# Kernel optimization log

Hardware: AMD Instinct MI355X
Metric: run time of the kernel (lower is better)

## Reference

```python
import jax, jax.numpy as jnp
import numpy as np

N_NODES = 100000
N_EDGES = 1600000
VOCAB = 128
D = 30
N_CLASSES = 5


def setup_inputs() -> dict:
    key = jax.random.key(0)
    ks = jax.random.split(key, 8)
    x = jax.random.randint(ks[0], (N_NODES,), 0, VOCAB)
    edge_index = jax.random.randint(ks[1], (2, N_EDGES), 0, N_NODES)
    emb = jax.random.normal(ks[2], (VOCAB, D), dtype=jnp.float32)
    W1 = jax.random.normal(ks[3], (D, D), dtype=jnp.float32) * (1.0 / np.sqrt(D))
    W2 = jax.random.normal(ks[4], (D, D), dtype=jnp.float32) * (1.0 / np.sqrt(D))
    W3 = jax.random.normal(ks[5], (D, D), dtype=jnp.float32) * (1.0 / np.sqrt(D))
    Wout = jax.random.normal(ks[6], (N_CLASSES, D), dtype=jnp.float32) * (1.0 / np.sqrt(D))
    b1 = jnp.zeros((D,), jnp.float32)
    b2 = jnp.zeros((D,), jnp.float32)
    b3 = jnp.zeros((D,), jnp.float32)
    bout = jnp.zeros((N_CLASSES,), jnp.float32)
    return dict(x=x, edge_index=edge_index, emb=emb, W1=W1, b1=b1, W2=W2, b2=b2,
                W3=W3, b3=b3, Wout=Wout, bout=bout)


def _gnn_layer(h, row, col, W, b):
    # h: [N, D]; row/col: [E+N] (self loops appended)
    n = h.shape[0]
    deg = jax.ops.segment_sum(jnp.ones(row.shape, h.dtype), row, num_segments=n)  # [N]
    msg = h[row] / deg[row][:, None]                 # gather + normalize: [E+N, D]
    agg = jax.ops.segment_sum(msg, col, num_segments=n)  # scatter-add: [N, D]
    return jax.nn.relu(agg @ W.T + b)


def reference(x, edge_index, emb, W1, b1, W2, b2, W3, b3, Wout, bout):
    n = x.shape[0]
    loops = jnp.arange(n, dtype=edge_index.dtype)
    row = jnp.concatenate([edge_index[0], loops])  # add_self_loops
    col = jnp.concatenate([edge_index[1], loops])
    h = emb[x]  # [N, D]
    for W, b in ((W1, b1), (W2, b2), (W3, b3)):
        h = _gnn_layer(h, row, col, W, b)
    return h @ Wout.T + bout  # [N, 5]
```

## Files before the change

### kernel.cpp

```cpp
#include <hip/hip_runtime.h>

#define D 30
#define DP 32
#define NCLS 5
#define VOCAB 128
#define BS 256
#define BSHIFT 8
#define BNODES 256
#define NSBMAX 512
#define CAP 8192
#define NBLK_S 256
#define CHUNK 6272
#define LDSCAP 6144
#define NPB 32


__global__ void k_init(int* __restrict__ gcur, int* __restrict__ rcur, int nsb) {
    int i = blockIdx.x * blockDim.x + threadIdx.x;
    if (i < nsb) { gcur[i] = i * CAP; rcur[i] = i * CAP; }
}

__global__ void __launch_bounds__(BS)
k_scatter3(const int* __restrict__ row, const int* __restrict__ col,
           int* __restrict__ gcur, int* __restrict__ rcur,
           int* __restrict__ ebuf, unsigned char* __restrict__ rbuf,
           int e, int nsb) {
    __shared__ int pay[CHUNK];
    __shared__ unsigned short bof[CHUNK];
    __shared__ int lhist[NSBMAX];
    __shared__ int lscan[NSBMAX];
    __shared__ int lcur[NSBMAX];
    __shared__ int gdst[NSBMAX];
    unsigned char* pay8 = (unsigned char*)pay;

    int per = (e + NBLK_S - 1) / NBLK_S;
    int s = blockIdx.x * per; if (s > e) s = e;
    int t = s + per; if (t > e) t = e;
    int m = t - s;
    int tid = threadIdx.x;

    for (int phase = 0; phase < 2; ++phase) {
        const int* key = phase == 0 ? col : row;
        lhist[tid] = 0; lhist[tid + 256] = 0;
        __syncthreads();
        for (int i = s + tid; i < t; i += BS)
            atomicAdd(&lhist[key[i] >> BSHIFT], 1);
        __syncthreads();
        lscan[tid] = lhist[tid]; lscan[tid + 256] = lhist[tid + 256];
        __syncthreads();
        for (int st = 1; st < NSBMAX; st <<= 1) {
            int t0 = (tid >= st) ? lscan[tid - st] : 0;
            int t1 = (tid + 256 >= st) ? lscan[tid + 256 - st] : 0;
            __syncthreads();
            lscan[tid] += t0; lscan[tid + 256] += t1;
            __syncthreads();
        }
        lcur[tid] = lscan[tid] - lhist[tid];
        lcur[tid + 256] = lscan[tid + 256] - lhist[tid + 256];
        __syncthreads();
        if (phase == 0) {
            for (int i = s + tid; i < t; i += BS) {
                int c = col[i], b = c >> BSHIFT;
                int p = atomicAdd(&lcur[b], 1);
                pay[p] = (row[i] << BSHIFT) | (c & (BNODES - 1));
                bof[p] = (unsigned short)b;
            }
        } else {
            for (int i = s + tid; i < t; i += BS) {
                int r = row[i], b = r >> BSHIFT;
                int p = atomicAdd(&lcur[b], 1);
                pay8[p] = (unsigned char)(r & (BNODES - 1));
                bof[p] = (unsigned short)b;
            }
        }
        __syncthreads();
        int* cur = phase == 0 ? gcur : rcur;
        for (int b = tid; b < nsb; b += BS) {
            int h = lhist[b];
            gdst[b] = h ? atomicAdd(&cur[b], h) : 0;
        }
        __syncthreads();
        if (phase == 0) {
            for (int p = tid; p < m; p += BS) {
                int b = bof[p];
                ebuf[gdst[b] + (p - (lscan[b] - lhist[b]))] = pay[p];
            }
        } else {
            for (int p = tid; p < m; p += BS) {
                int b = bof[p];
                rbuf[gdst[b] + (p - (lscan[b] - lhist[b]))] = pay8[p];
            }
        }
        __syncthreads();
    }
}

__global__ void __launch_bounds__(BS)
k_odbsort(int* __restrict__ ebuf, const unsigned char* __restrict__ rbuf,
          const int* __restrict__ gcur, const int* __restrict__ rcur,
          const int* __restrict__ x, float* __restrict__ rdeg, int2* __restrict__ xr,
          int* __restrict__ off, int* __restrict__ cnt, int n) {
    __shared__ int ledge[LDSCAP];
    __shared__ int c256[BNODES];
    __shared__ int b256[BNODES];
    __shared__ int cur256[BNODES];
    int bkt = blockIdx.x;
    int tid = threadIdx.x;
    int base = bkt * CAP;
    int rm = rcur[bkt] - base;
    c256[tid] = 0;
    __syncthreads();
    for (int k = tid; k < rm; k += BS)
        atomicAdd(&c256[rbuf[base + k]], 1);
    __syncthreads();
    {
        int node = (bkt << BSHIFT) + tid;
        if (node < n) {
            float rd = 1.0f / (float)(c256[tid] + 1);
            rdeg[node] = rd;
            xr[node] = make_int2(x[node], __float_as_int(rd));
        }
    }
    __syncthreads();
    int m = gcur[bkt] - base;
    if (m > LDSCAP) m = LDSCAP;
    for (int k = tid; k < m; k += BS) ledge[k] = ebuf[base + k];
    c256[tid] = 0;
    __syncthreads();
    for (int k = tid; k < m; k += BS)
        atomicAdd(&c256[ledge[k] & (BNODES - 1)], 1);
    __syncthreads();
    b256[tid] = c256[tid];
    __syncthreads();
    for (int st = 1; st < BNODES; st <<= 1) {
        int tv = (tid >= st) ? b256[tid - st] : 0;
        __syncthreads();
        b256[tid] += tv;
        __syncthreads();
    }
    cur256[tid] = b256[tid] - c256[tid];
    {
        int node = (bkt << BSHIFT) + tid;
        if (node < n) {
            off[node] = base + b256[tid] - c256[tid];
            cnt[node] = c256[tid];
        }
    }
    __syncthreads();
    for (int k = tid; k < m; k += BS) {
        int v = ledge[k];
        int p = atomicAdd(&cur256[v & (BNODES - 1)], 1);
        ebuf[base + p] = v >> BSHIFT;
    }
}

__global__ void k_prep_emb(const float* __restrict__ emb, float* __restrict__ embp) {
    int tid = blockIdx.x * blockDim.x + threadIdx.x;
    if (tid >= VOCAB * DP) return;
    int v = tid >> 5, c = tid & (DP - 1);
    embp[tid] = (c < D) ? emb[v * D + c] : 0.0f;
}

__global__ void __launch_bounds__(BS)
k_agg_lin(const float* __restrict__ Ain, const int2* __restrict__ xr,
          const float* __restrict__ embp,
          const int* __restrict__ off, const int* __restrict__ cnt,
          const int* __restrict__ esrc, const float* __restrict__ rdeg,
          const float* __restrict__ W, const float* __restrict__ bias,
          const float* __restrict__ Wout, const float* __restrict__ bout,
          float* __restrict__ Aout, float* __restrict__ out,
          int n, int srcmode, int outmode) {
    __shared__ float aggS[NPB * DP];
    __shared__ float h3S[NPB * D];
    __shared__ float Ws[D * D];
    __shared__ float bs_[D];
    __shared__ float WoS[NCLS * D];
    __shared__ float boS[NCLS];
    const float4* Ain4  = (const float4*)Ain;
    const float4* embp4 = (const float4*)embp;
    int i0 = blockIdx.x * NPB;
    int j = threadIdx.x >> 3;
    int q = threadIdx.x & 7;
    int i = i0 + j;
    for (int p = threadIdx.x; p < D * D; p += BS) Ws[p] = W[p];
    if (threadIdx.x < D) bs_[threadIdx.x] = bias[threadIdx.x];
    if (outmode == 1) {
        for (int p = threadIdx.x; p < NCLS * D; p += BS) WoS[p] = Wout[p];
        if (threadIdx.x < NCLS) boS[threadIdx.x] = bout[threadIdx.x];
    }
    float ax = 0.0f, ay = 0.0f, az = 0.0f, aw = 0.0f;
    if (i < n) {
        int base = off[i], c = cnt[i], k = 0;
        if (srcmode == 0) {
            float4 sv = Ain4[(size_t)i * 8 + q];
            ax = sv.x; ay = sv.y; az = sv.z; aw = sv.w;
            for (; k + 8 <= c; k += 8) {
                int s0 = esrc[base + k + 0], s1 = esrc[base + k + 1];
                int s2 = esrc[base + k + 2], s3 = esrc[base + k + 3];
                int s4 = esrc[base + k + 4], s5 = esrc[base + k + 5];
                int s6 = esrc[base + k + 6], s7 = esrc[base + k + 7];
                float4 a0 = Ain4[(size_t)s0 * 8 + q];
                float4 a1 = Ain4[(size_t)s1 * 8 + q];
                float4 a2 = Ain4[(size_t)s2 * 8 + q];
                float4 a3 = Ain4[(size_t)s3 * 8 + q];
                float4 a4 = Ain4[(size_t)s4 * 8 + q];
                float4 a5 = Ain4[(size_t)s5 * 8 + q];
                float4 a6 = Ain4[(size_t)s6 * 8 + q];
                float4 a7 = Ain4[(size_t)s7 * 8 + q];
                ax += a0.x; ay += a0.y; az += a0.z; aw += a0.w;
                ax += a1.x; ay += a1.y; az += a1.z; aw += a1.w;
                ax += a2.x; ay += a2.y; az += a2.z; aw += a2.w;
                ax += a3.x; ay += a3.y; az += a3.z; aw += a3.w;
                ax += a4.x; ay += a4.y; az += a4.z; aw += a4.w;
                ax += a5.x; ay += a5.y; az += a5.z; aw += a5.w;
                ax += a6.x; ay += a6.y; az += a6.z; aw += a6.w;
                ax += a7.x; ay += a7.y; az += a7.z; aw += a7.w;
            }
            for (; k < c; ++k) {
                float4 a = Ain4[(size_t)esrc[base + k] * 8 + q];
                ax += a.x; ay += a.y; az += a.z; aw += a.w;
            }
        } else {
            int2 xi = xr[i];
            float ri = __int_as_float(xi.y);
            float4 ev = embp4[(size_t)xi.x * 8 + q];
            ax = ev.x * ri; ay = ev.y * ri; az = ev.z * ri; aw = ev.w * ri;
            for (; k + 4 <= c; k += 4) {
                int s0 = esrc[base + k + 0], s1 = esrc[base + k + 1];
                int s2 = esrc[base + k + 2], s3 = esrc[base + k + 3];
                int2 x0 = xr[s0], x1 = xr[s1], x2 = xr[s2], x3 = xr[s3];
                float4 e0 = embp4[(size_t)x0.x * 8 + q];
                float4 e1 = embp4[(size_t)x1.x * 8 + q];
                float4 e2 = embp4[(size_t)x2.x * 8 + q];
                float4 e3 = embp4[(size_t)x3.x * 8 + q];
                float r0 = __int_as_float(x0.y), r1 = __int_as_float(x1.y);
                float r2 = __int_as_float(x2.y), r3 = __int_as_float(x3.y);
                ax = fmaf(e0.x, r0, ax); ay = fmaf(e0.y, r0, ay);
                az = fmaf(e0.z, r0, az); aw = fmaf(e0.w, r0, aw);
                ax = fmaf(e1.x, r1, ax); ay = fmaf(e1.y, r1, ay);
                az = fmaf(e1.z, r1, az); aw = fmaf(e1.w, r1, aw);
                ax = fmaf(e2.x, r2, ax); ay = fmaf(e2.y, r2, ay);
                az = fmaf(e2.z, r2, az); aw = fmaf(e2.w, r2, aw);
                ax = fmaf(e3.x, r3, ax); ay = fmaf(e3.y, r3, ay);
                az = fmaf(e3.z, r3, az); aw = fmaf(e3.w, r3, aw);
            }
            for (; k < c; ++k) {
                int2 xs = xr[esrc[base + k]];
                float rr = __int_as_float(xs.y);
                float4 e = embp4[(size_t)xs.x * 8 + q];
                ax = fmaf(e.x, rr, ax); ay = fmaf(e.y, rr, ay);
                az = fmaf(e.z, rr, az); aw = fmaf(e.w, rr, aw);
            }
        }
    }
    ((float4*)aggS)[j * 8 + q] = make_float4(ax, ay, az, aw);
    __syncthreads();
    if (outmode == 0) {
        for (int it = threadIdx.x; it < NPB * DP; it += BS) {
            int jj = it >> 5, cc = it & (DP - 1);
            int nd = i0 + jj;
            if (nd >= n) continue;
            float a = 0.0f;
            if (cc < D) {
                a = bs_[cc];
                const float* ar = &aggS[jj * DP];
                const float* wr = &Ws[cc * D];
#pragma unroll
                for (int dd = 0; dd < D; ++dd) a = fmaf(ar[dd], wr[dd], a);
                a = fmaxf(a, 0.0f) * rdeg[nd];
            }
            Aout[(size_t)nd * DP + cc] = a;
        }
    } else {
        for (int it = threadIdx.x; it < NPB * D; it += BS) {
            int jj = it / D, cc = it - jj * D;
            float a = bs_[cc];
            const float* ar = &aggS[jj * DP];
            const float* wr = &Ws[cc * D];
#pragma unroll
            for (int dd = 0; dd < D; ++dd) a = fmaf(ar[dd], wr[dd], a);
            h3S[it] = fmaxf(a, 0.0f);
        }
        __syncthreads();
        for (int it = threadIdx.x; it < NPB * NCLS; it += BS) {
            int jj = it / NCLS, cc = it - jj * NCLS;
            int nd = i0 + jj;
            if (nd >= n) continue;
            float a = boS[cc];
            const float* hr = &h3S[jj * D];
            const float* wr = &WoS[cc * D];
#pragma unroll
            for (int dd = 0; dd < D; ++dd) a = fmaf(hr[dd], wr[dd], a);
            out[(size_t)nd * NCLS + cc] = a;
        }
    }
}


extern "C" void kernel_launch(void* const* d_in, const int* in_sizes, int n_in,
                              void* d_out, int out_size, void* d_ws, size_t ws_size,
                              hipStream_t stream) {
    const int*   x    = (const int*)d_in[0];
    const int*   ei   = (const int*)d_in[1];
    const float* emb  = (const float*)d_in[2];
    const float* W1   = (const float*)d_in[3];
    const float* b1   = (const float*)d_in[4];
    const float* W2   = (const float*)d_in[5];
    const float* b2   = (const float*)d_in[6];
    const float* W3   = (const float*)d_in[7];
    const float* b3   = (const float*)d_in[8];
    const float* Wout = (const float*)d_in[9];
    const float* bout = (const float*)d_in[10];
    float* out = (float*)d_out;

    const int N = in_sizes[0];
    const int E = in_sizes[1] / 2;
    const int* row = ei;
    const int* col = ei + E;
    const int nsb = (N + BNODES - 1) >> BSHIFT;

    float* A0   = (float*)d_ws;
    float* A1   = A0 + (size_t)N * DP;
    float* embp = A1 + (size_t)N * DP;
    float* rdeg = embp + VOCAB * DP;
    int2*  xr   = (int2*)(rdeg + N);
    int*   ebuf = (int*)(xr + N);
    unsigned char* rbuf = (unsigned char*)(ebuf + (size_t)nsb * CAP);
    int*   off  = (int*)(rbuf + (((size_t)nsb * CAP + 3) & ~(size_t)3));
    int*   cnt  = off + N;
    int*   gcur = cnt + N;
    int*   rcur = gcur + nsb;

    dim3 blk(BS);

    k_init<<<dim3((nsb + BS - 1) / BS), blk, 0, stream>>>(gcur, rcur, nsb);
    k_scatter3<<<dim3(NBLK_S), blk, 0, stream>>>(row, col, gcur, rcur,
                                                 ebuf, rbuf, E, nsb);
    k_odbsort<<<dim3(nsb), blk, 0, stream>>>(ebuf, rbuf, gcur, rcur, x,
                                             rdeg, xr, off, cnt, N);
    k_prep_emb<<<dim3((VOCAB * DP + BS - 1) / BS), blk, 0, stream>>>(emb, embp);

    dim3 gAgg((N + NPB - 1) / NPB);
    k_agg_lin<<<gAgg, blk, 0, stream>>>(nullptr, xr, embp, off, cnt, ebuf, rdeg,
                                        W1, b1, Wout, bout, A1, out, N, 1, 0);
    k_agg_lin<<<gAgg, blk, 0, stream>>>(A1, xr, embp, off, cnt, ebuf, rdeg,
                                        W2, b2, Wout, bout, A0, out, N, 0, 0);
    k_agg_lin<<<gAgg, blk, 0, stream>>>(A0, xr, embp, off, cnt, ebuf, rdeg,
                                        W3, b3, Wout, bout, A1, out, N, 0, 1);
}
```

Before: 244.3 us.

## Use 128-node buckets with more scatter blocks and merge prep kernels

Halves the bucket size from 256 to 128 nodes, which doubles the number of buckets to about 782, and quadruples the scatter grid to 1024 blocks with smaller per-block chunks. The point is to raise parallelism and occupancy in the edge binning and per-bucket sort stages. It also folds the embedding padding into the cursor init kernel, removing one launch. The cost is a 1024-entry histogram and scan per scatter block, and half-idle threads in the sort kernel.

Measured after the change: 267.3 us. 1.09x slower.

```diff
diff --git a/kernel.cpp b/kernel.cpp
--- a/kernel.cpp
+++ b/kernel.cpp
@@ -5,19 +5,24 @@
 #define NCLS 5
 #define VOCAB 128
 #define BS 256
-#define BSHIFT 8
-#define BNODES 256
-#define NSBMAX 512
-#define CAP 8192
-#define NBLK_S 256
-#define CHUNK 6272
-#define LDSCAP 6144
+#define BSHIFT 7
+#define BNODES 128
+#define NSB2 1024
+#define CAP 4096
+#define NBLK_S 1024
+#define CHUNK 1568
+#define LDSCAP 3072
 #define NPB 32
 
 
-__global__ void k_init(int* __restrict__ gcur, int* __restrict__ rcur, int nsb) {
+__global__ void k_prep(int* __restrict__ gcur, int* __restrict__ rcur, int nsb,
+                       const float* __restrict__ emb, float* __restrict__ embp) {
     int i = blockIdx.x * blockDim.x + threadIdx.x;
     if (i < nsb) { gcur[i] = i * CAP; rcur[i] = i * CAP; }
+    if (i < VOCAB * DP) {
+        int v = i >> 5, c = i & (DP - 1);
+        embp[i] = (c < D) ? emb[v * D + c] : 0.0f;
+    }
 }
 
 __global__ void __launch_bounds__(BS)
@@ -27,10 +32,10 @@
            int e, int nsb) {
     __shared__ int pay[CHUNK];
     __shared__ unsigned short bof[CHUNK];
-    __shared__ int lhist[NSBMAX];
-    __shared__ int lscan[NSBMAX];
-    __shared__ int lcur[NSBMAX];
-    __shared__ int gdst[NSBMAX];
+    __shared__ int lhist[NSB2];
+    __shared__ int lscan[NSB2];
+    __shared__ int lcur[NSB2];
+    __shared__ int gdst[NSB2];
     unsigned char* pay8 = (unsigned char*)pay;
 
     int per = (e + NBLK_S - 1) / NBLK_S;
@@ -41,22 +46,32 @@
 
     for (int phase = 0; phase < 2; ++phase) {
         const int* key = phase == 0 ? col : row;
-        lhist[tid] = 0; lhist[tid + 256] = 0;
+#pragma unroll
+        for (int u = 0; u < 4; ++u) lhist[tid + u * 256] = 0;
         __syncthreads();
         for (int i = s + tid; i < t; i += BS)
             atomicAdd(&lhist[key[i] >> BSHIFT], 1);
         __syncthreads();
-        lscan[tid] = lhist[tid]; lscan[tid + 256] = lhist[tid + 256];
-        __syncthreads();
-        for (int st = 1; st < NSBMAX; st <<= 1) {
-            int t0 = (tid >= st) ? lscan[tid - st] : 0;
-            int t1 = (tid + 256 >= st) ? lscan[tid + 256 - st] : 0;
+#pragma unroll
+        for (int u = 0; u < 4; ++u) lscan[tid + u * 256] = lhist[tid + u * 256];
+        __syncthreads();
+        for (int st = 1; st < NSB2; st <<= 1) {
+            int tv[4];
+#pragma unroll
+            for (int u = 0; u < 4; ++u) {
+                int idx = tid + u * 256;
+                tv[u] = (idx >= st) ? lscan[idx - st] : 0;
+            }
             __syncthreads();
-            lscan[tid] += t0; lscan[tid + 256] += t1;
+#pragma unroll
+            for (int u = 0; u < 4; ++u) lscan[tid + u * 256] += tv[u];
             __syncthreads();
         }
-        lcur[tid] = lscan[tid] - lhist[tid];
-        lcur[tid + 256] = lscan[tid + 256] - lhist[tid + 256];
+#pragma unroll
+        for (int u = 0; u < 4; ++u) {
+            int idx = tid + u * 256;
+            lcur[idx] = lscan[idx] - lhist[idx];
+        }
         __syncthreads();
         if (phase == 0) {
             for (int i = s + tid; i < t; i += BS) {
@@ -101,22 +116,22 @@
           const int* __restrict__ x, float* __restrict__ rdeg, int2* __restrict__ xr,
           int* __restrict__ off, int* __restrict__ cnt, int n) {
     __shared__ int ledge[LDSCAP];
-    __shared__ int c256[BNODES];
-    __shared__ int b256[BNODES];
-    __shared__ int cur256[BNODES];
+    __shared__ int c128[BNODES];
+    __shared__ int b128[BNODES];
+    __shared__ int cur128[BNODES];
     int bkt = blockIdx.x;
     int tid = threadIdx.x;
     int base = bkt * CAP;
     int rm = rcur[bkt] - base;
-    c256[tid] = 0;
+    if (tid < BNODES) c128[tid] = 0;
     __syncthreads();
     for (int k = tid; k < rm; k += BS)
-        atomicAdd(&c256[rbuf[base + k]], 1);
-    __syncthreads();
-    {
+        atomicAdd(&c128[rbuf[base + k]], 1);
+    __syncthreads();
+    if (tid < BNODES) {
         int node = (bkt << BSHIFT) + tid;
         if (node < n) {
-            float rd = 1.0f / (float)(c256[tid] + 1);
+            float rd = 1.0f / (float)(c128[tid] + 1);
             rdeg[node] = rd;
             xr[node] = make_int2(x[node], __float_as_int(rd));
         }
@@ -125,40 +140,33 @@
     int m = gcur[bkt] - base;
     if (m > LDSCAP) m = LDSCAP;
     for (int k = tid; k < m; k += BS) ledge[k] = ebuf[base + k];
-    c256[tid] = 0;
+    if (tid < BNODES) c128[tid] = 0;
     __syncthreads();
     for (int k = tid; k < m; k += BS)
-        atomicAdd(&c256[ledge[k] & (BNODES - 1)], 1);
-    __syncthreads();
-    b256[tid] = c256[tid];
+        atomicAdd(&c128[ledge[k] & (BNODES - 1)], 1);
+    __syncthreads();
+    if (tid < BNODES) b128[tid] = c128[tid];
     __syncthreads();
     for (int st = 1; st < BNODES; st <<= 1) {
-        int tv = (tid >= st) ? b256[tid - st] : 0;
-        __syncthreads();
-        b256[tid] += tv;
-        __syncthreads();
-    }
-    cur256[tid] = b256[tid] - c256[tid];
-    {
+        int tv = (tid >= st && tid < BNODES) ? b128[tid - st] : 0;
+        __syncthreads();
+        if (tid < BNODES) b128[tid] += tv;
+        __syncthreads();
+    }
+    if (tid < BNODES) {
+        cur128[tid] = b128[tid] - c128[tid];
         int node = (bkt << BSHIFT) + tid;
         if (node < n) {
-            off[node] = base + b256[tid] - c256[tid];
-            cnt[node] = c256[tid];
+            off[node] = base + b128[tid] - c128[tid];
+            cnt[node] = c128[tid];
         }
     }
     __syncthreads();
     for (int k = tid; k < m; k += BS) {
         int v = ledge[k];
-        int p = atomicAdd(&cur256[v & (BNODES - 1)], 1);
+        int p = atomicAdd(&cur128[v & (BNODES - 1)], 1);
         ebuf[base + p] = v >> BSHIFT;
     }
-}
-
-__global__ void k_prep_emb(const float* __restrict__ emb, float* __restrict__ embp) {
-    int tid = blockIdx.x * blockDim.x + threadIdx.x;
-    if (tid >= VOCAB * DP) return;
-    int v = tid >> 5, c = tid & (DP - 1);
-    embp[tid] = (c < D) ? emb[v * D + c] : 0.0f;
 }
 
 __global__ void __launch_bounds__(BS)
@@ -333,12 +341,11 @@
 
     dim3 blk(BS);
 
-    k_init<<<dim3((nsb + BS - 1) / BS), blk, 0, stream>>>(gcur, rcur, nsb);
+    k_prep<<<dim3((VOCAB * DP + BS - 1) / BS), blk, 0, stream>>>(gcur, rcur, nsb, emb, embp);
     k_scatter3<<<dim3(NBLK_S), blk, 0, stream>>>(row, col, gcur, rcur,
                                                  ebuf, rbuf, E, nsb);
     k_odbsort<<<dim3(nsb), blk, 0, stream>>>(ebuf, rbuf, gcur, rcur, x,
                                              rdeg, xr, off, cnt, N);
-    k_prep_emb<<<dim3((VOCAB * DP + BS - 1) / BS), blk, 0, stream>>>(emb, embp);
 
     dim3 gAgg((N + NPB - 1) / NPB);
     k_agg_lin<<<gAgg, blk, 0, stream>>>(nullptr, xr, embp, off, cnt, ebuf, rdeg,
```

## Split scatter and bucket-sort phases across separate blocks, merge init kernels

Applied to the files above, without the earlier changes.

The two sequential phases of the scatter kernel (col-keyed and row-keyed) now run in separate blocks of a doubled grid, each with 512 threads. The degree-count and edge-sort halves of the bucket kernel also run in separate blocks. The init and embedding-padding kernels are merged into one launch. The aim is more parallel blocks on the preprocessing stages and one fewer launch, at the cost of more blocks contending for global atomics and the loss of the per-block shared-memory reuse between phases.

Result: faster. 226.0 us (-7.5%).

```diff
diff --git a/kernel.cpp b/kernel.cpp
--- a/kernel.cpp
+++ b/kernel.cpp
@@ -5,6 +5,7 @@
 #define NCLS 5
 #define VOCAB 128
 #define BS 256
+#define BSS 512
 #define BSHIFT 8
 #define BNODES 256
 #define NSBMAX 512
@@ -15,12 +16,17 @@
 #define NPB 32
 
 
-__global__ void k_init(int* __restrict__ gcur, int* __restrict__ rcur, int nsb) {
+__global__ void k_prep(int* __restrict__ gcur, int* __restrict__ rcur, int nsb,
+                       const float* __restrict__ emb, float* __restrict__ embp) {
     int i = blockIdx.x * blockDim.x + threadIdx.x;
     if (i < nsb) { gcur[i] = i * CAP; rcur[i] = i * CAP; }
-}
-
-__global__ void __launch_bounds__(BS)
+    if (i < VOCAB * DP) {
+        int v = i >> 5, c = i & (DP - 1);
+        embp[i] = (c < D) ? emb[v * D + c] : 0.0f;
+    }
+}
+
+__global__ void __launch_bounds__(BSS)
 k_scatter3(const int* __restrict__ row, const int* __restrict__ col,
            int* __restrict__ gcur, int* __restrict__ rcur,
            int* __restrict__ ebuf, unsigned char* __restrict__ rbuf,
@@ -33,65 +39,62 @@
     __shared__ int gdst[NSBMAX];
     unsigned char* pay8 = (unsigned char*)pay;
 
+    int phase = blockIdx.x >= NBLK_S;
+    int blk = blockIdx.x - phase * NBLK_S;
+    const int* key = phase ? row : col;
     int per = (e + NBLK_S - 1) / NBLK_S;
-    int s = blockIdx.x * per; if (s > e) s = e;
+    int s = blk * per; if (s > e) s = e;
     int t = s + per; if (t > e) t = e;
     int m = t - s;
     int tid = threadIdx.x;
 
-    for (int phase = 0; phase < 2; ++phase) {
-        const int* key = phase == 0 ? col : row;
-        lhist[tid] = 0; lhist[tid + 256] = 0;
-        __syncthreads();
-        for (int i = s + tid; i < t; i += BS)
-            atomicAdd(&lhist[key[i] >> BSHIFT], 1);
-        __syncthreads();
-        lscan[tid] = lhist[tid]; lscan[tid + 256] = lhist[tid + 256];
-        __syncthreads();
-        for (int st = 1; st < NSBMAX; st <<= 1) {
-            int t0 = (tid >= st) ? lscan[tid - st] : 0;
-            int t1 = (tid + 256 >= st) ? lscan[tid + 256 - st] : 0;
-            __syncthreads();
-            lscan[tid] += t0; lscan[tid + 256] += t1;
-            __syncthreads();
-        }
-        lcur[tid] = lscan[tid] - lhist[tid];
-        lcur[tid + 256] = lscan[tid + 256] - lhist[tid + 256];
-        __syncthreads();
-        if (phase == 0) {
-            for (int i = s + tid; i < t; i += BS) {
-                int c = col[i], b = c >> BSHIFT;
-                int p = atomicAdd(&lcur[b], 1);
-                pay[p] = (row[i] << BSHIFT) | (c & (BNODES - 1));
-                bof[p] = (unsigned short)b;
-            }
-        } else {
-            for (int i = s + tid; i < t; i += BS) {
-                int r = row[i], b = r >> BSHIFT;
-                int p = atomicAdd(&lcur[b], 1);
-                pay8[p] = (unsigned char)(r & (BNODES - 1));
-                bof[p] = (unsigned short)b;
-            }
-        }
-        __syncthreads();
-        int* cur = phase == 0 ? gcur : rcur;
-        for (int b = tid; b < nsb; b += BS) {
-            int h = lhist[b];
-            gdst[b] = h ? atomicAdd(&cur[b], h) : 0;
-        }
-        __syncthreads();
-        if (phase == 0) {
-            for (int p = tid; p < m; p += BS) {
-                int b = bof[p];
-                ebuf[gdst[b] + (p - (lscan[b] - lhist[b]))] = pay[p];
-            }
-        } else {
-            for (int p = tid; p < m; p += BS) {
-                int b = bof[p];
-                rbuf[gdst[b] + (p - (lscan[b] - lhist[b]))] = pay8[p];
-            }
-        }
-        __syncthreads();
+    lhist[tid] = 0;
+    __syncthreads();
+    for (int i = s + tid; i < t; i += BSS)
+        atomicAdd(&lhist[key[i] >> BSHIFT], 1);
+    __syncthreads();
+    lscan[tid] = lhist[tid];
+    __syncthreads();
+    for (int st = 1; st < NSBMAX; st <<= 1) {
+        int tv = (tid >= st) ? lscan[tid - st] : 0;
+        __syncthreads();
+        lscan[tid] += tv;
+        __syncthreads();
+    }
+    lcur[tid] = lscan[tid] - lhist[tid];
+    __syncthreads();
+    if (phase == 0) {
+        for (int i = s + tid; i < t; i += BSS) {
+            int c = col[i], b = c >> BSHIFT;
+            int p = atomicAdd(&lcur[b], 1);
+            pay[p] = (row[i] << BSHIFT) | (c & (BNODES - 1));
+            bof[p] = (unsigned short)b;
+        }
+    } else {
+        for (int i = s + tid; i < t; i += BSS) {
+            int r = row[i], b = r >> BSHIFT;
+            int p = atomicAdd(&lcur[b], 1);
+            pay8[p] = (unsigned char)(r & (BNODES - 1));
+            bof[p] = (unsigned short)b;
+        }
+    }
+    __syncthreads();
+    int* cur = phase ? rcur : gcur;
+    if (tid < nsb) {
+        int h = lhist[tid];
+        gdst[tid] = h ? atomicAdd(&cur[tid], h) : 0;
+    }
+    __syncthreads();
+    if (phase == 0) {
+        for (int p = tid; p < m; p += BSS) {
+            int b = bof[p];
+            ebuf[gdst[b] + (p - (lscan[b] - lhist[b]))] = pay[p];
+        }
+    } else {
+        for (int p = tid; p < m; p += BSS) {
+            int b = bof[p];
+            rbuf[gdst[b] + (p - (lscan[b] - lhist[b]))] = pay8[p];
+        }
     }
 }
 
@@ -99,66 +102,59 @@
 k_odbsort(int* __restrict__ ebuf, const unsigned char* __restrict__ rbuf,
           const int* __restrict__ gcur, const int* __restrict__ rcur,
           const int* __restrict__ x, float* __restrict__ rdeg, int2* __restrict__ xr,
-          int* __restrict__ off, int* __restrict__ cnt, int n) {
+          int* __restrict__ off, int* __restrict__ cnt, int n, int nsb) {
     __shared__ int ledge[LDSCAP];
     __shared__ int c256[BNODES];
     __shared__ int b256[BNODES];
     __shared__ int cur256[BNODES];
-    int bkt = blockIdx.x;
+    int side = blockIdx.x >= nsb;
+    int bkt = side ? blockIdx.x - nsb : blockIdx.x;
     int tid = threadIdx.x;
     int base = bkt * CAP;
-    int rm = rcur[bkt] - base;
-    c256[tid] = 0;
-    __syncthreads();
-    for (int k = tid; k < rm; k += BS)
-        atomicAdd(&c256[rbuf[base + k]], 1);
-    __syncthreads();
-    {
+
+    if (side == 0) {
+        int rm = rcur[bkt] - base;
+        c256[tid] = 0;
+        __syncthreads();
+        for (int k = tid; k < rm; k += BS)
+            atomicAdd(&c256[rbuf[base + k]], 1);
+        __syncthreads();
         int node = (bkt << BSHIFT) + tid;
         if (node < n) {
             float rd = 1.0f / (float)(c256[tid] + 1);
             rdeg[node] = rd;
             xr[node] = make_int2(x[node], __float_as_int(rd));
         }
-    }
-    __syncthreads();
-    int m = gcur[bkt] - base;
-    if (m > LDSCAP) m = LDSCAP;
-    for (int k = tid; k < m; k += BS) ledge[k] = ebuf[base + k];
-    c256[tid] = 0;
-    __syncthreads();
-    for (int k = tid; k < m; k += BS)
-        atomicAdd(&c256[ledge[k] & (BNODES - 1)], 1);
-    __syncthreads();
-    b256[tid] = c256[tid];
-    __syncthreads();
-    for (int st = 1; st < BNODES; st <<= 1) {
-        int tv = (tid >= st) ? b256[tid - st] : 0;
-        __syncthreads();
-        b256[tid] += tv;
-        __syncthreads();
-    }
-    cur256[tid] = b256[tid] - c256[tid];
-    {
+    } else {
+        int m = gcur[bkt] - base;
+        if (m > LDSCAP) m = LDSCAP;
+        for (int k = tid; k < m; k += BS) ledge[k] = ebuf[base + k];
+        c256[tid] = 0;
+        __syncthreads();
+        for (int k = tid; k < m; k += BS)
+            atomicAdd(&c256[ledge[k] & (BNODES - 1)], 1);
+        __syncthreads();
+        b256[tid] = c256[tid];
+        __syncthreads();
+        for (int st = 1; st < BNODES; st <<= 1) {
+            int tv = (tid >= st) ? b256[tid - st] : 0;
+            __syncthreads();
+            b256[tid] += tv;
+            __syncthreads();
+        }
+        cur256[tid] = b256[tid] - c256[tid];
         int node = (bkt << BSHIFT) + tid;
         if (node < n) {
             off[node] = base + b256[tid] - c256[tid];
             cnt[node] = c256[tid];
         }
-    }
-    __syncthreads();
-    for (int k = tid; k < m; k += BS) {
-        int v = ledge[k];
-        int p = atomicAdd(&cur256[v & (BNODES - 1)], 1);
-        ebuf[base + p] = v >> BSHIFT;
-    }
-}
-
-__global__ void k_prep_emb(const float* __restrict__ emb, float* __restrict__ embp) {
-    int tid = blockIdx.x * blockDim.x + threadIdx.x;
-    if (tid >= VOCAB * DP) return;
-    int v = tid >> 5, c = tid & (DP - 1);
-    embp[tid] = (c < D) ? emb[v * D + c] : 0.0f;
+        __syncthreads();
+        for (int k = tid; k < m; k += BS) {
+            int v = ledge[k];
+            int p = atomicAdd(&cur256[v & (BNODES - 1)], 1);
+            ebuf[base + p] = v >> BSHIFT;
+        }
+    }
 }
 
 __global__ void __launch_bounds__(BS)
@@ -333,12 +329,11 @@
 
     dim3 blk(BS);
 
-    k_init<<<dim3((nsb + BS - 1) / BS), blk, 0, stream>>>(gcur, rcur, nsb);
-    k_scatter3<<<dim3(NBLK_S), blk, 0, stream>>>(row, col, gcur, rcur,
-                                                 ebuf, rbuf, E, nsb);
-    k_odbsort<<<dim3(nsb), blk, 0, stream>>>(ebuf, rbuf, gcur, rcur, x,
-                                             rdeg, xr, off, cnt, N);
-    k_prep_emb<<<dim3((VOCAB * DP + BS - 1) / BS), blk, 0, stream>>>(emb, embp);
+    k_prep<<<dim3((VOCAB * DP + BS - 1) / BS), blk, 0, stream>>>(gcur, rcur, nsb, emb, embp);
+    k_scatter3<<<dim3(2 * NBLK_S), dim3(BSS), 0, stream>>>(row, col, gcur, rcur,
+                                                           ebuf, rbuf, E, nsb);
+    k_odbsort<<<dim3(2 * nsb), blk, 0, stream>>>(ebuf, rbuf, gcur, rcur, x,
+                                                 rdeg, xr, off, cnt, N, nsb);
 
     dim3 gAgg((N + NPB - 1) / NPB);
     k_agg_lin<<<gAgg, blk, 0, stream>>>(nullptr, xr, embp, off, cnt, ebuf, rdeg,
```
